# Kernel tuning notes

Measured on AMD Instinct MI355X. Metric: run time of the kernel, lower is better.

Reference implementation:

```python
import jax, jax.numpy as jnp
import numpy as np


def setup_inputs() -> dict:
    key = jax.random.key(0)
    k1, k2, k3, k4, k5 = jax.random.split(key, 5)
    B, S, IN, OUT, GS = 64, 1, 8192, 28672, 128
    n_groups = IN // GS  # 64
    return {
        "input": jax.random.normal(k1, (B, S, IN), dtype=jnp.float32),
        # packed int4 weights: two 4-bit values per byte along in_features
        "qweight": jax.random.randint(k2, (IN // 2, OUT), 0, 256, dtype=jnp.int32),
        # per-group scales (small positive, typical of quantized weights)
        "scales": (jax.random.uniform(k3, (n_groups, OUT), dtype=jnp.float32) * 0.01 + 1e-3),
        # per-group zero points, 4-bit range
        "qzeros": jax.random.randint(k4, (n_groups, OUT), 0, 16, dtype=jnp.int32),
        "bias": jax.random.normal(k5, (OUT,), dtype=jnp.float32),
        "group_size": GS,
    }


def _dequant_int4(qweight, scales, qzeros, group_size):
    # qweight: [in/2, out] bytes; low nibble = even k, high nibble = odd k
    half_in, out_f = qweight.shape
    in_f = half_in * 2
    lo = qweight & 0xF
    hi = (qweight >> 4) & 0xF
    # interleave nibbles along in_features -> [in, out]
    w_q = jnp.stack([lo, hi], axis=1).reshape(in_f, out_f).astype(scales.dtype)
    n_groups = scales.shape[0]
    # (q - zero) * scale, per group of `group_size` rows
    w = (w_q.reshape(n_groups, group_size, out_f)
         - qzeros.astype(scales.dtype)[:, None, :]) * scales[:, None, :]
    return w.reshape(in_f, out_f)


def reference(input, qweight, scales, qzeros, bias, group_size):
    # Fused dequant-int4 matmul (decode path, seq_len == 1): y = x @ W + b
    w = _dequant_int4(qweight, scales, qzeros, group_size)  # [in, out]
    return jnp.einsum('bsi,io->bso', input, w) + bias
```

## Files before the change

kernel.cpp:

```cpp
#include <hip/hip_runtime.h>
#include <hip/hip_bf16.h>


typedef float  f32x4 __attribute__((ext_vector_type(4)));
typedef short  s16x8 __attribute__((ext_vector_type(8)));
typedef int    i32x4 __attribute__((ext_vector_type(4)));

#define K_DIM  8192
#define N_DIM  28672
#define BN     64
#define CK     128
#define NCHUNK (K_DIM / CK)

__device__ s16x8 g_wsa[NCHUNK * 1024];

static __device__ __forceinline__ short f2bf(float f) {
    return (short)__builtin_bit_cast(unsigned short, __float2bfloat16(f));
}

__global__ __launch_bounds__(256)
void prep_a_kernel(const float* __restrict__ x) {
    const int tid = threadIdx.x;
    const int c   = blockIdx.x >> 2;
    const int mb  = blockIdx.x & 3;
    const int k8  = tid & 15;
    const int m   = mb * 16 + (tid >> 4);
    const float* src = x + (size_t)m * K_DIM + c * CK + k8 * 8;
    f32x4 a = *(const f32x4*)src;
    f32x4 b = *(const f32x4*)(src + 4);
    s16x8 o;
    o[0] = f2bf(a[0]); o[1] = f2bf(a[1]); o[2] = f2bf(a[2]); o[3] = f2bf(a[3]);
    o[4] = f2bf(b[0]); o[5] = f2bf(b[1]); o[6] = f2bf(b[2]); o[7] = f2bf(b[3]);
    g_wsa[(size_t)c * 1024 + k8 * 64 + m] = o;
}

__global__ __launch_bounds__(256, 3)
void int4gemm_kernel(const int*   __restrict__ qw,
                     const float* __restrict__ sc,
                     const int*   __restrict__ qz,
                     const float* __restrict__ bias,
                     float*       __restrict__ out)
{
    __shared__ s16x8 lB[2][16 * 64];

    const int tid   = threadIdx.x;
    const int lane  = tid & 63;
    const int w     = tid >> 6;
    const int nbase = blockIdx.x * BN;

    const int col = lane;

    const int l15 = lane & 15;
    const int lk  = lane >> 4;
    const int mh  = w >> 1;
    const int nh  = w & 1;

    const int*   qcol = qw + nbase + col;
    const float* scol = sc + nbase + col;
    const int*   zcol = qz + nbase + col;

    f32x4 acc[2][2];
#pragma unroll
    for (int mi = 0; mi < 2; ++mi)
#pragma unroll
        for (int ni = 0; ni < 2; ++ni) acc[mi][ni] = (f32x4)0.0f;

    int   bvC[16], bvN[16];
    float sC, sN_;
    int   zC, zN_;

#pragma unroll
    for (int u = 0; u < 16; ++u)
        bvC[u] = qcol[(size_t)(16 * w + u) * N_DIM];
    sC = scol[0];
    zC = zcol[0];

    const i32x4* wsa  = (const i32x4*)g_wsa;
    const int    aoff = lk * 64 + mh * 32 + l15;

    for (int c = 0; c < NCHUNK; ++c) {
        const int cb = (c + 1) & (NCHUNK - 1);

#pragma unroll
        for (int u = 0; u < 16; ++u)
            bvN[u] = qcol[(size_t)(cb * 64 + 16 * w + u) * N_DIM];
        sN_ = scol[(size_t)cb * N_DIM];
        zN_ = zcol[(size_t)cb * N_DIM];

        i32x4 af[4][2];
#pragma unroll
        for (int ks = 0; ks < 4; ++ks)
#pragma unroll
            for (int mi = 0; mi < 2; ++mi)
                af[ks][mi] = wsa[(size_t)c * 1024 + ks * 256 + mi * 16 + aoff];

        const float s = sC;
        const float o = -(float)zC * s;
#pragma unroll
        for (int jp = 0; jp < 4; ++jp) {
            s16x8 cell;
#pragma unroll
            for (int uu = 0; uu < 4; ++uu) {
                const int v = bvC[4 * jp + uu];
                cell[2 * uu]     = f2bf(fmaf((float)(v & 15), s, o));
                cell[2 * uu + 1] = f2bf(fmaf((float)(v >> 4), s, o));
            }
            lB[c & 1][(4 * w + jp) * 64 + col] = cell;
        }

        asm volatile("s_waitcnt lgkmcnt(0)" ::: "memory");
        asm volatile("s_barrier" ::: "memory");

#pragma unroll
        for (int ks = 0; ks < 4; ++ks) {
            const int cidx = (ks * 4 + lk) * 64 + nh * 32 + l15;
            const s16x8 b0 = lB[c & 1][cidx];
            const s16x8 b1 = lB[c & 1][cidx + 16];
#pragma unroll
            for (int mi = 0; mi < 2; ++mi) {
                const s16x8 a = __builtin_bit_cast(s16x8, af[ks][mi]);
                acc[mi][0] = __builtin_amdgcn_mfma_f32_16x16x32_bf16(a, b0, acc[mi][0], 0, 0, 0);
                acc[mi][1] = __builtin_amdgcn_mfma_f32_16x16x32_bf16(a, b1, acc[mi][1], 0, 0, 0);
            }
        }

#pragma unroll
        for (int u = 0; u < 16; ++u) bvC[u] = bvN[u];
        sC = sN_;
        zC = zN_;
    }

#pragma unroll
    for (int ni = 0; ni < 2; ++ni) {
        const int   ncol = nbase + nh * 32 + ni * 16 + l15;
        const float bv   = bias[ncol];
#pragma unroll
        for (int mi = 0; mi < 2; ++mi) {
#pragma unroll
            for (int jj = 0; jj < 4; ++jj) {
                const int m = mh * 32 + mi * 16 + lk * 4 + jj;
                out[(size_t)m * N_DIM + ncol] = acc[mi][ni][jj] + bv;
            }
        }
    }
}

extern "C" void kernel_launch(void* const* d_in, const int* in_sizes, int n_in,
                              void* d_out, int out_size, void* d_ws, size_t ws_size,
                              hipStream_t stream) {
    const float* x    = (const float*)d_in[0];
    const int*   qw   = (const int*)d_in[1];
    const float* sc   = (const float*)d_in[2];
    const int*   qz   = (const int*)d_in[3];
    const float* bias = (const float*)d_in[4];
    float*       out  = (float*)d_out;

    prep_a_kernel<<<dim3(256), dim3(256), 0, stream>>>(x);
    int4gemm_kernel<<<dim3(N_DIM / BN), dim3(256), 0, stream>>>(qw, sc, qz, bias, out);
}
```

Before: 143.6 us.

## Dequantize int4 in registers via bf16 magic-number trick and factor out scale/zero

Removes the LDS staging and barrier for dequantized weights: each wave now loads its own packed weights into registers and forms bf16 B fragments directly with a 0x4380 exponent-bias trick, so no per-element convert or fma is needed. Scale and zero-point are applied after each group's MFMA through a per-group row-sum of the activations computed in the prep kernel, which subtracts the zero-point term. Loads switch to raw buffer intrinsics, and the occupancy hint in launch bounds is dropped. Each wave now reloads duplicated weights, and the larger register footprint may reduce occupancy.

```diff
diff --git a/kernel.cpp b/kernel.cpp
--- a/kernel.cpp
+++ b/kernel.cpp
@@ -10,12 +10,25 @@
 #define N_DIM  28672
 #define BN     64
 #define CK     128
-#define NCHUNK (K_DIM / CK)
+#define NCHUNK 64
+#define ROWB   (N_DIM * 4)
 
 __device__ s16x8 g_wsa[NCHUNK * 1024];
+__device__ float g_rowsum[NCHUNK * 64];
+
+__device__ int   llvm_amdgcn_raw_buffer_load_i32(i32x4 srsrc, int voff, int soff, int aux) __asm("llvm.amdgcn.raw.buffer.load.i32");
+__device__ f32x4 llvm_amdgcn_raw_buffer_load_v4f32(i32x4 srsrc, int voff, int soff, int aux) __asm("llvm.amdgcn.raw.buffer.load.v4f32");
 
 static __device__ __forceinline__ short f2bf(float f) {
     return (short)__builtin_bit_cast(unsigned short, __float2bfloat16(f));
+}
+static __device__ __forceinline__ float bf2f(short s) {
+    return __builtin_bit_cast(float, ((unsigned)(unsigned short)s) << 16);
+}
+static __device__ __forceinline__ i32x4 make_srsrc(const void* p, unsigned bytes) {
+    union { struct { const void* ptr; unsigned rec; unsigned cfg; } s; i32x4 v; } u;
+    u.s.ptr = p; u.s.rec = bytes; u.s.cfg = 0x00020000;
+    return u.v;
 }
 
 __global__ __launch_bounds__(256)
@@ -32,32 +45,39 @@
     o[0] = f2bf(a[0]); o[1] = f2bf(a[1]); o[2] = f2bf(a[2]); o[3] = f2bf(a[3]);
     o[4] = f2bf(b[0]); o[5] = f2bf(b[1]); o[6] = f2bf(b[2]); o[7] = f2bf(b[3]);
     g_wsa[(size_t)c * 1024 + k8 * 64 + m] = o;
+    float ps = 0.f;
+#pragma unroll
+    for (int j = 0; j < 8; ++j) ps += bf2f(o[j]);
+    ps += __shfl_xor(ps, 1);
+    ps += __shfl_xor(ps, 2);
+    ps += __shfl_xor(ps, 4);
+    ps += __shfl_xor(ps, 8);
+    if (k8 == 0) g_rowsum[c * 64 + m] = ps;
 }
 
-__global__ __launch_bounds__(256, 3)
+__global__ __launch_bounds__(256)
 void int4gemm_kernel(const int*   __restrict__ qw,
                      const float* __restrict__ sc,
                      const int*   __restrict__ qz,
                      const float* __restrict__ bias,
                      float*       __restrict__ out)
 {
-    __shared__ s16x8 lB[2][16 * 64];
-
     const int tid   = threadIdx.x;
     const int lane  = tid & 63;
     const int w     = tid >> 6;
     const int nbase = blockIdx.x * BN;
-
-    const int col = lane;
 
     const int l15 = lane & 15;
     const int lk  = lane >> 4;
     const int mh  = w >> 1;
     const int nh  = w & 1;
 
-    const int*   qcol = qw + nbase + col;
-    const float* scol = sc + nbase + col;
-    const int*   zcol = qz + nbase + col;
+    const i32x4 srA = make_srsrc((const void*)g_wsa, NCHUNK * 1024 * 16);
+    const i32x4 srB = make_srsrc((const void*)qw, 4096u * (unsigned)ROWB);
+
+    const int voffA = (lk * 64 + mh * 32 + l15) * 16;
+    const int voffB = (lk * 4) * ROWB + (nbase + nh * 32 + l15) * 4;
+    const int ncol0 = nbase + nh * 32 + l15;
 
     f32x4 acc[2][2];
 #pragma unroll
@@ -65,81 +85,100 @@
 #pragma unroll
         for (int ni = 0; ni < 2; ++ni) acc[mi][ni] = (f32x4)0.0f;
 
-    int   bvC[16], bvN[16];
-    float sC, sN_;
-    int   zC, zN_;
+    int bvC[32], bvN[32];
 
 #pragma unroll
-    for (int u = 0; u < 16; ++u)
-        bvC[u] = qcol[(size_t)(16 * w + u) * N_DIM];
-    sC = scol[0];
-    zC = zcol[0];
+    for (int ks = 0; ks < 4; ++ks)
+#pragma unroll
+        for (int nti = 0; nti < 2; ++nti)
+#pragma unroll
+            for (int d = 0; d < 4; ++d)
+                bvC[(ks * 2 + nti) * 4 + d] =
+                    llvm_amdgcn_raw_buffer_load_i32(srB, voffB + nti * 64,
+                                                    (ks * 16 + d) * ROWB, 0);
 
-    const i32x4* wsa  = (const i32x4*)g_wsa;
-    const int    aoff = lk * 64 + mh * 32 + l15;
-
+#pragma unroll 2
     for (int c = 0; c < NCHUNK; ++c) {
-        const int cb = (c + 1) & (NCHUNK - 1);
-
-#pragma unroll
-        for (int u = 0; u < 16; ++u)
-            bvN[u] = qcol[(size_t)(cb * 64 + 16 * w + u) * N_DIM];
-        sN_ = scol[(size_t)cb * N_DIM];
-        zN_ = zcol[(size_t)cb * N_DIM];
-
-        i32x4 af[4][2];
+        f32x4 af[8];
 #pragma unroll
         for (int ks = 0; ks < 4; ++ks)
 #pragma unroll
             for (int mi = 0; mi < 2; ++mi)
-                af[ks][mi] = wsa[(size_t)c * 1024 + ks * 256 + mi * 16 + aoff];
+                af[ks * 2 + mi] = llvm_amdgcn_raw_buffer_load_v4f32(
+                    srA, voffA + mi * 256, c * 16384 + ks * 4096, 0);
+        const float s0 = sc[(size_t)c * N_DIM + ncol0];
+        const float s1 = sc[(size_t)c * N_DIM + ncol0 + 16];
+        const int   z0 = qz[(size_t)c * N_DIM + ncol0];
+        const int   z1 = qz[(size_t)c * N_DIM + ncol0 + 16];
+        const f32x4 rs0 = *(const f32x4*)&g_rowsum[c * 64 + mh * 32 + lk * 4];
+        const f32x4 rs1 = *(const f32x4*)&g_rowsum[c * 64 + mh * 32 + 16 + lk * 4];
 
-        const float s = sC;
-        const float o = -(float)zC * s;
+        __builtin_amdgcn_sched_barrier(0);
+
+        const int cb = (c + 1) & (NCHUNK - 1);
 #pragma unroll
-        for (int jp = 0; jp < 4; ++jp) {
-            s16x8 cell;
+        for (int ks = 0; ks < 4; ++ks)
 #pragma unroll
-            for (int uu = 0; uu < 4; ++uu) {
-                const int v = bvC[4 * jp + uu];
-                cell[2 * uu]     = f2bf(fmaf((float)(v & 15), s, o));
-                cell[2 * uu + 1] = f2bf(fmaf((float)(v >> 4), s, o));
+            for (int nti = 0; nti < 2; ++nti)
+#pragma unroll
+                for (int d = 0; d < 4; ++d)
+                    bvN[(ks * 2 + nti) * 4 + d] =
+                        llvm_amdgcn_raw_buffer_load_i32(srB, voffB + nti * 64,
+                                                        (cb * 64 + ks * 16 + d) * ROWB, 0);
+
+        s16x8 bf[8];
+#pragma unroll
+        for (int fi = 0; fi < 8; ++fi) {
+            i32x4 f;
+#pragma unroll
+            for (int d = 0; d < 4; ++d) {
+                const int v = bvC[fi * 4 + d];
+                f[d] = 0x43804380 | (v & 15) | ((v >> 4) << 16);
             }
-            lB[c & 1][(4 * w + jp) * 64 + col] = cell;
+            bf[fi] = __builtin_bit_cast(s16x8, f);
         }
 
-        asm volatile("s_waitcnt lgkmcnt(0)" ::: "memory");
-        asm volatile("s_barrier" ::: "memory");
-
+        f32x4 pc[2][2];
+#pragma unroll
+        for (int mi = 0; mi < 2; ++mi)
+#pragma unroll
+            for (int ni = 0; ni < 2; ++ni) pc[mi][ni] = (f32x4)0.0f;
 #pragma unroll
         for (int ks = 0; ks < 4; ++ks) {
-            const int cidx = (ks * 4 + lk) * 64 + nh * 32 + l15;
-            const s16x8 b0 = lB[c & 1][cidx];
-            const s16x8 b1 = lB[c & 1][cidx + 16];
 #pragma unroll
             for (int mi = 0; mi < 2; ++mi) {
-                const s16x8 a = __builtin_bit_cast(s16x8, af[ks][mi]);
-                acc[mi][0] = __builtin_amdgcn_mfma_f32_16x16x32_bf16(a, b0, acc[mi][0], 0, 0, 0);
-                acc[mi][1] = __builtin_amdgcn_mfma_f32_16x16x32_bf16(a, b1, acc[mi][1], 0, 0, 0);
+                const s16x8 a = __builtin_bit_cast(s16x8, af[ks * 2 + mi]);
+                pc[mi][0] = __builtin_amdgcn_mfma_f32_16x16x32_bf16(a, bf[ks * 2 + 0], pc[mi][0], 0, 0, 0);
+                pc[mi][1] = __builtin_amdgcn_mfma_f32_16x16x32_bf16(a, bf[ks * 2 + 1], pc[mi][1], 0, 0, 0);
+            }
+        }
+
+        const float h0 = 0.5f * s0, w0 = s0 * (128.0f + (float)z0);
+        const float h1 = 0.5f * s1, w1 = s1 * (128.0f + (float)z1);
+#pragma unroll
+        for (int mi = 0; mi < 2; ++mi) {
+            const f32x4 rs = mi ? rs1 : rs0;
+#pragma unroll
+            for (int j = 0; j < 4; ++j) {
+                acc[mi][0][j] = fmaf(pc[mi][0][j], h0, fmaf(rs[j], -w0, acc[mi][0][j]));
+                acc[mi][1][j] = fmaf(pc[mi][1][j], h1, fmaf(rs[j], -w1, acc[mi][1][j]));
             }
         }
 
 #pragma unroll
-        for (int u = 0; u < 16; ++u) bvC[u] = bvN[u];
-        sC = sN_;
-        zC = zN_;
+        for (int u = 0; u < 32; ++u) bvC[u] = bvN[u];
     }
 
 #pragma unroll
-    for (int ni = 0; ni < 2; ++ni) {
-        const int   ncol = nbase + nh * 32 + ni * 16 + l15;
+    for (int nti = 0; nti < 2; ++nti) {
+        const int   ncol = ncol0 + nti * 16;
         const float bv   = bias[ncol];
 #pragma unroll
         for (int mi = 0; mi < 2; ++mi) {
 #pragma unroll
-            for (int jj = 0; jj < 4; ++jj) {
-                const int m = mh * 32 + mi * 16 + lk * 4 + jj;
-                out[(size_t)m * N_DIM + ncol] = acc[mi][ni][jj] + bv;
+            for (int j = 0; j < 4; ++j) {
+                const int m = mh * 32 + mi * 16 + lk * 4 + j;
+                out[(size_t)m * N_DIM + ncol] = acc[mi][nti][j] + bv;
             }
         }
     }
```

After: 180.9 us. 26.0% more time.

## Double work-group to 512 threads with two-chunk-deep weight prefetch and buffer loads

Applied to the files above, without the earlier changes.

Each block now runs 8 waves instead of 4, so each wave dequantizes 8 packed rows per chunk instead of 16 and computes a single 16-column MFMA tile. Weight, scale and zero-point prefetch moves from one chunk ahead to two chunks ahead, with sched_barriers to keep the loads issued early. Activation fragments are read with raw buffer loads. The aim is more memory requests in flight and more occupancy to hide latency in this bandwidth-bound decode GEMM, at the cost of extra registers and more barrier participants per block.

```diff
diff --git a/kernel.cpp b/kernel.cpp
--- a/kernel.cpp
+++ b/kernel.cpp
@@ -10,12 +10,19 @@
 #define N_DIM  28672
 #define BN     64
 #define CK     128
-#define NCHUNK (K_DIM / CK)
+#define NCHUNK 64
 
 __device__ s16x8 g_wsa[NCHUNK * 1024];
 
+__device__ f32x4 llvm_amdgcn_raw_buffer_load_v4f32(i32x4 srsrc, int voff, int soff, int aux) __asm("llvm.amdgcn.raw.buffer.load.v4f32");
+
 static __device__ __forceinline__ short f2bf(float f) {
     return (short)__builtin_bit_cast(unsigned short, __float2bfloat16(f));
+}
+static __device__ __forceinline__ i32x4 make_srsrc(const void* p, unsigned bytes) {
+    union { struct { const void* ptr; unsigned rec; unsigned cfg; } s; i32x4 v; } u;
+    u.s.ptr = p; u.s.rec = bytes; u.s.cfg = 0x00020000;
+    return u.v;
 }
 
 __global__ __launch_bounds__(256)
@@ -34,7 +41,7 @@
     g_wsa[(size_t)c * 1024 + k8 * 64 + m] = o;
 }
 
-__global__ __launch_bounds__(256, 3)
+__global__ __launch_bounds__(512, 4)
 void int4gemm_kernel(const int*   __restrict__ qw,
                      const float* __restrict__ sc,
                      const int*   __restrict__ qz,
@@ -48,99 +55,95 @@
     const int w     = tid >> 6;
     const int nbase = blockIdx.x * BN;
 
-    const int col = lane;
-
-    const int l15 = lane & 15;
-    const int lk  = lane >> 4;
-    const int mh  = w >> 1;
-    const int nh  = w & 1;
-
+    const int col  = lane;
     const int*   qcol = qw + nbase + col;
     const float* scol = sc + nbase + col;
     const int*   zcol = qz + nbase + col;
 
-    f32x4 acc[2][2];
-#pragma unroll
-    for (int mi = 0; mi < 2; ++mi)
-#pragma unroll
-        for (int ni = 0; ni < 2; ++ni) acc[mi][ni] = (f32x4)0.0f;
+    const int l15 = lane & 15;
+    const int lk  = lane >> 4;
+    const int mh  = w >> 2;
+    const int wn  = (w & 3) * 16;
 
-    int   bvC[16], bvN[16];
-    float sC, sN_;
-    int   zC, zN_;
+    const i32x4 srA  = make_srsrc((const void*)g_wsa, NCHUNK * 1024 * 16);
+    const int   voffA = (lk * 64 + mh * 32 + l15) * 16;
+
+    f32x4 acc[2];
+    acc[0] = (f32x4)0.0f;
+    acc[1] = (f32x4)0.0f;
+
+    int   bvC[8], bvB[8], bvN[8];
+    float sC, sB_, sN_;
+    int   zC, zB_, zN_;
 
 #pragma unroll
-    for (int u = 0; u < 16; ++u)
-        bvC[u] = qcol[(size_t)(16 * w + u) * N_DIM];
-    sC = scol[0];
-    zC = zcol[0];
+    for (int u = 0; u < 8; ++u) {
+        bvC[u] = qcol[(size_t)(8 * w + u) * N_DIM];
+        bvB[u] = qcol[(size_t)(64 + 8 * w + u) * N_DIM];
+    }
+    sC  = scol[0];               zC  = zcol[0];
+    sB_ = scol[N_DIM];           zB_ = zcol[N_DIM];
 
-    const i32x4* wsa  = (const i32x4*)g_wsa;
-    const int    aoff = lk * 64 + mh * 32 + l15;
-
+#pragma unroll 2
     for (int c = 0; c < NCHUNK; ++c) {
-        const int cb = (c + 1) & (NCHUNK - 1);
-
-#pragma unroll
-        for (int u = 0; u < 16; ++u)
-            bvN[u] = qcol[(size_t)(cb * 64 + 16 * w + u) * N_DIM];
-        sN_ = scol[(size_t)cb * N_DIM];
-        zN_ = zcol[(size_t)cb * N_DIM];
-
-        i32x4 af[4][2];
+        f32x4 af[8];
 #pragma unroll
         for (int ks = 0; ks < 4; ++ks)
 #pragma unroll
             for (int mi = 0; mi < 2; ++mi)
-                af[ks][mi] = wsa[(size_t)c * 1024 + ks * 256 + mi * 16 + aoff];
+                af[ks * 2 + mi] = llvm_amdgcn_raw_buffer_load_v4f32(
+                    srA, voffA + mi * 256, c * 16384 + ks * 4096, 0);
+        __builtin_amdgcn_sched_barrier(0);
+
+        const int cb = (c + 2) & (NCHUNK - 1);
+#pragma unroll
+        for (int u = 0; u < 8; ++u)
+            bvN[u] = qcol[(size_t)(cb * 64 + 8 * w + u) * N_DIM];
+        sN_ = scol[(size_t)cb * N_DIM];
+        zN_ = zcol[(size_t)cb * N_DIM];
+        __builtin_amdgcn_sched_barrier(0);
 
         const float s = sC;
         const float o = -(float)zC * s;
+        s16x8 c0, c1;
 #pragma unroll
-        for (int jp = 0; jp < 4; ++jp) {
-            s16x8 cell;
-#pragma unroll
-            for (int uu = 0; uu < 4; ++uu) {
-                const int v = bvC[4 * jp + uu];
-                cell[2 * uu]     = f2bf(fmaf((float)(v & 15), s, o));
-                cell[2 * uu + 1] = f2bf(fmaf((float)(v >> 4), s, o));
-            }
-            lB[c & 1][(4 * w + jp) * 64 + col] = cell;
+        for (int uu = 0; uu < 4; ++uu) {
+            const int v0 = bvC[uu];
+            const int v1 = bvC[4 + uu];
+            c0[2 * uu]     = f2bf(fmaf((float)(v0 & 15), s, o));
+            c0[2 * uu + 1] = f2bf(fmaf((float)(v0 >> 4), s, o));
+            c1[2 * uu]     = f2bf(fmaf((float)(v1 & 15), s, o));
+            c1[2 * uu + 1] = f2bf(fmaf((float)(v1 >> 4), s, o));
         }
+        lB[c & 1][(2 * w) * 64 + col]     = c0;
+        lB[c & 1][(2 * w + 1) * 64 + col] = c1;
 
         asm volatile("s_waitcnt lgkmcnt(0)" ::: "memory");
         asm volatile("s_barrier" ::: "memory");
 
 #pragma unroll
         for (int ks = 0; ks < 4; ++ks) {
-            const int cidx = (ks * 4 + lk) * 64 + nh * 32 + l15;
-            const s16x8 b0 = lB[c & 1][cidx];
-            const s16x8 b1 = lB[c & 1][cidx + 16];
-#pragma unroll
-            for (int mi = 0; mi < 2; ++mi) {
-                const s16x8 a = __builtin_bit_cast(s16x8, af[ks][mi]);
-                acc[mi][0] = __builtin_amdgcn_mfma_f32_16x16x32_bf16(a, b0, acc[mi][0], 0, 0, 0);
-                acc[mi][1] = __builtin_amdgcn_mfma_f32_16x16x32_bf16(a, b1, acc[mi][1], 0, 0, 0);
-            }
+            const s16x8 bfr = lB[c & 1][(ks * 4 + lk) * 64 + wn + l15];
+            const s16x8 a0  = __builtin_bit_cast(s16x8, af[ks * 2 + 0]);
+            const s16x8 a1  = __builtin_bit_cast(s16x8, af[ks * 2 + 1]);
+            acc[0] = __builtin_amdgcn_mfma_f32_16x16x32_bf16(a0, bfr, acc[0], 0, 0, 0);
+            acc[1] = __builtin_amdgcn_mfma_f32_16x16x32_bf16(a1, bfr, acc[1], 0, 0, 0);
         }
 
 #pragma unroll
-        for (int u = 0; u < 16; ++u) bvC[u] = bvN[u];
-        sC = sN_;
-        zC = zN_;
+        for (int u = 0; u < 8; ++u) { bvC[u] = bvB[u]; bvB[u] = bvN[u]; }
+        sC = sB_; sB_ = sN_;
+        zC = zB_; zB_ = zN_;
     }
 
+    const int   ncol = nbase + wn + l15;
+    const float bv   = bias[ncol];
 #pragma unroll
-    for (int ni = 0; ni < 2; ++ni) {
-        const int   ncol = nbase + nh * 32 + ni * 16 + l15;
-        const float bv   = bias[ncol];
+    for (int mi = 0; mi < 2; ++mi) {
 #pragma unroll
-        for (int mi = 0; mi < 2; ++mi) {
-#pragma unroll
-            for (int jj = 0; jj < 4; ++jj) {
-                const int m = mh * 32 + mi * 16 + lk * 4 + jj;
-                out[(size_t)m * N_DIM + ncol] = acc[mi][ni][jj] + bv;
-            }
+        for (int j = 0; j < 4; ++j) {
+            const int m = mh * 32 + mi * 16 + lk * 4 + j;
+            out[(size_t)m * N_DIM + ncol] = acc[mi][j] + bv;
         }
     }
 }
@@ -156,5 +159,5 @@
     float*       out  = (float*)d_out;
 
     prep_a_kernel<<<dim3(256), dim3(256), 0, stream>>>(x);
-    int4gemm_kernel<<<dim3(N_DIM / BN), dim3(256), 0, stream>>>(qw, sc, qz, bias, out);
+    int4gemm_kernel<<<dim3(N_DIM / BN), dim3(512), 0, stream>>>(qw, sc, qz, bias, out);
 }
```

After: 146.7 us. +2.2%, slower.
